# Performance work log

Hardware: AMD Instinct MI355X
Metric: run time of the kernel (lower is better)

Reference implementation:

```python
import jax, jax.numpy as jnp
import numpy as np

T, N, HID = 128, 128, 64
H_, W_ = 8, 8
CONV_OUT = H_ * W_ * HID  # 4096
N_SUB = 5
A, B, C = 5, 3, 6          # subtask_space = task_space.nvec[0]
SUB_SIZE = A + B + C       # 14
N_G = A * B * C            # 90
STATE = N_SUB + SUB_SIZE + HID + SUB_SIZE + 1 + 1  # 99
D_IN = CONV_OUT + 3 * N_SUB  # 4111


def setup_inputs() -> dict:
    key = jax.random.key(0)
    ks = jax.random.split(key, 16)
    sc = 0.02
    obs = jax.random.normal(ks[0], (T, N, CONV_OUT), jnp.float32)
    task_type = jax.random.randint(ks[1], (T, N, N_SUB), 0, A).astype(jnp.float32)
    count = jax.random.randint(ks[2], (T, N, N_SUB), 1, B + 1).astype(jnp.float32)
    obj = jax.random.randint(ks[3], (T, N, N_SUB), 0, C).astype(jnp.float32)
    inp = jnp.concatenate([obs, task_type, count, obj], axis=-1)  # [T,N,4111]
    hx = jnp.zeros((1, N, STATE), jnp.float32)
    return {
        "input": inp,
        "hx": hx,
        "Wf": jax.random.normal(ks[4], (HID, CONV_OUT + 2 * SUB_SIZE + 1), jnp.float32) * sc,
        "bf": jnp.zeros((HID,), jnp.float32),
        "Wih": jax.random.normal(ks[5], (3 * HID, 2 * HID), jnp.float32) * sc,
        "bih": jnp.zeros((3 * HID,), jnp.float32),
        "bhh": jnp.zeros((3 * HID,), jnp.float32),
        "Wc": jax.random.normal(ks[6], (1, 2 * HID), jnp.float32) * sc,
        "bc": jnp.zeros((1,), jnp.float32),
        "Wl": jax.random.normal(ks[7], (3, HID), jnp.float32) * sc,
        "bl": jnp.zeros((3,), jnp.float32),
        "Wpi": jax.random.normal(ks[8], (N_G, HID + SUB_SIZE), jnp.float32) * sc,
        "bpi": jnp.zeros((N_G,), jnp.float32),
        "Wb": jax.random.normal(ks[9], (2, CONV_OUT + SUB_SIZE), jnp.float32) * sc,
        "bb": jnp.zeros((2,), jnp.float32),
    }


def _forward(input, hx, Wf, bf, Wih, bih, bhh, Wc, bc, Wl, bl, Wpi, bpi, Wb, bb):
    obs = input[..., :CONV_OUT]
    tt = input[..., CONV_OUT:CONV_OUT + N_SUB].astype(jnp.int32)
    cnt = input[..., CONV_OUT + N_SUB:CONV_OUT + 2 * N_SUB].astype(jnp.int32) - 1
    obj = input[..., CONV_OUT + 2 * N_SUB:].astype(jnp.int32)

    ea, eb, ec = jnp.eye(A, dtype=input.dtype), jnp.eye(B, dtype=input.dtype), jnp.eye(C, dtype=input.dtype)

    def embed(t1, t2, t3):
        return jnp.concatenate([ea[t1], eb[t2], ec[t3]], axis=-1)

    M = embed(tt[0], cnt[0], obj[0])  # [N, N_SUB, SUB_SIZE]

    # parse hidden state
    h0_all = hx[0]
    i0, i1, i2, i3, i4 = np.cumsum([N_SUB, SUB_SIZE, HID, SUB_SIZE, 1])
    p0, r0, h0, g0, b0 = (h0_all[:, :i0], h0_all[:, i0:i1], h0_all[:, i1:i2],
                          h0_all[:, i2:i3], h0_all[:, i3:i4])

    new_ep = jnp.all(hx == 0)
    p0 = jnp.where(new_ep, p0.at[:, 0].set(1.0), p0)
    r0 = jnp.where(new_ep, M[:, 0], r0)
    g0 = jnp.where(new_ep, M[:, 0], g0)

    bhr, bhz, bhn = jnp.split(bhh, 3)
    keys = jax.random.split(jax.random.key(42), input.shape[0])

    def step(carry, xs):
        p_, r_, h_, g_, bprev = carry
        x, k = xs
        s = jnp.concatenate([x, r_, g_, bprev], axis=-1) @ Wf.T + bf   # f (linear)
        sh = jnp.concatenate([s, h_], axis=-1)
        cg = jax.nn.sigmoid(sh @ Wc.T + bc)                             # [N,1] phi_update
        # GRUCell called with hidden=None -> zero hidden state
        gi = sh @ Wih.T + bih
        gr, gz, gn = jnp.split(gi, 3, axis=-1)
        rg = jax.nn.sigmoid(gr + bhr)
        z = jax.nn.sigmoid(gz + bhz)
        n = jnp.tanh(gn + rg * bhn)
        hnew = (1.0 - z) * n
        # shift attention: per-batch conv1d(p, l, padding=1)
        l = jax.nn.softmax(h_ @ Wl.T + bl, axis=-1)                     # [N,3]
        pp = jnp.pad(p_, ((0, 0), (1, 1)))
        pconv = pp[:, :-2] * l[:, :1] + pp[:, 1:-1] * l[:, 1:2] + pp[:, 2:] * l[:, 2:]
        rnew = jnp.einsum('nk,nks->ns', pconv, M)
        p = cg * pconv + (1.0 - cg) * p_
        r = cg * rnew + (1.0 - cg) * r_
        h = cg * hnew + (1.0 - cg) * h_
        # pi_theta categorical over prod(subtask_space)
        lg = jnp.concatenate([h, r], axis=-1) @ Wpi.T + bpi
        k1, k2 = jax.random.split(k)
        g_idx = jax.random.categorical(k1, lg)                          # [N]
        lp_g = jnp.take_along_axis(jax.nn.log_softmax(lg, axis=-1), g_idx[:, None], axis=1)
        t1 = g_idx // (B * C)
        rem = g_idx % (B * C)
        gemb = embed(t1, rem // C, rem % C)                             # [N, SUB_SIZE]
        g = cg * gemb + (1.0 - cg) * g_
        # beta categorical over 2
        lbeta = jnp.concatenate([x, g], axis=-1) @ Wb.T + bb
        b_idx = jax.random.categorical(k2, lbeta)
        lp_b = jnp.take_along_axis(jax.nn.log_softmax(lbeta, axis=-1), b_idx[:, None], axis=1)
        bflt = b_idx[:, None].astype(p.dtype)
        out = jnp.concatenate([p, r, h, g, bflt, lp_g + lp_b], axis=-1)  # [N, STATE]
        return (p, r, h, g, bflt), out

    _, outs = jax.lax.scan(step, (p0, r0, h0, g0, b0), (obs, keys))
    return outs  # [T, N, STATE]


def reference(input, hx, Wf, bf, Wih, bih, bhh, Wc, bc, Wl, bl, Wpi, bpi, Wb, bb):
    outs = _forward(input, hx, Wf, bf, Wih, bih, bhh, Wc, bc, Wl, bl, Wpi, bpi, Wb, bb)
    return outs, outs[-1]
```

## Files before the change

kernel.cpp:

```cpp
#include <hip/hip_runtime.h>
#include <stdint.h>
#include <math.h>

#define T_STEPS 128
#define NB      128
#define HID     64
#define CONVOUT 4096
#define NSUB    5
#define SUBSZ   14
#define NG      90
#define STATE   99
#define DIN     4111
#define WFCOLS  4125
#define WBCOLS  4110
#define NROWS   (T_STEPS * NB)

__device__ __forceinline__ void tf2x32(unsigned k0, unsigned k1,
                                       unsigned x0, unsigned x1,
                                       unsigned &o0, unsigned &o1) {
  unsigned K0 = k0, K1 = k1, K2 = k0 ^ k1 ^ 0x1BD11BDAu;
  x0 += K0; x1 += K1;
  const int R0[4] = {13, 15, 26, 6};
  const int R1[4] = {17, 29, 16, 24};
  #pragma unroll
  for (int j = 0; j < 4; ++j) { x0 += x1; x1 = (x1 << R0[j]) | (x1 >> (32 - R0[j])); x1 ^= x0; }
  x0 += K1; x1 += K2 + 1u;
  #pragma unroll
  for (int j = 0; j < 4; ++j) { x0 += x1; x1 = (x1 << R1[j]) | (x1 >> (32 - R1[j])); x1 ^= x0; }
  x0 += K2; x1 += K0 + 2u;
  #pragma unroll
  for (int j = 0; j < 4; ++j) { x0 += x1; x1 = (x1 << R0[j]) | (x1 >> (32 - R0[j])); x1 ^= x0; }
  x0 += K0; x1 += K1 + 3u;
  #pragma unroll
  for (int j = 0; j < 4; ++j) { x0 += x1; x1 = (x1 << R1[j]) | (x1 >> (32 - R1[j])); x1 ^= x0; }
  x0 += K1; x1 += K2 + 4u;
  #pragma unroll
  for (int j = 0; j < 4; ++j) { x0 += x1; x1 = (x1 << R0[j]) | (x1 >> (32 - R0[j])); x1 ^= x0; }
  x0 += K2; x1 += K0 + 5u;
  o0 = x0; o1 = x1;
}

__device__ __forceinline__ double bits_to_gumbel_d(unsigned bits) {
  float f = __uint_as_float((bits >> 9) | 0x3f800000u) - 1.0f;
  const double tiny = (double)1.17549435e-38f;
  double u = fmax(tiny, (double)f + tiny);
  return -log(-log(u));
}

__device__ __forceinline__ float rlane(float v, int l) {
  return __int_as_float(__builtin_amdgcn_readlane(__float_as_int(v), l));
}

__device__ __forceinline__ void bar_lds() {
  __asm__ volatile("" ::: "memory");
  __builtin_amdgcn_s_waitcnt(0xC07F);
  __builtin_amdgcn_s_barrier();
  __asm__ volatile("" ::: "memory");
}

__global__ void k_transpose(const float* __restrict__ Wf, const float* __restrict__ Wb,
                            float* __restrict__ Wt) {
  int idx = blockIdx.x * 256 + threadIdx.x;
  int c = idx >> 12;
  int k = idx & 4095;
  float v = (c < 64) ? Wf[(size_t)c * WFCOLS + k] : Wb[(size_t)(c - 64) * WBCOLS + k];
  Wt[(size_t)k * 68 + c] = v;
}

__global__ __launch_bounds__(256, 4) void k_gemm(const float* __restrict__ inp,
                                                 const float* __restrict__ Wt,
                                                 float* __restrict__ Pf,
                                                 double* __restrict__ Pd) {
  __shared__ __align__(16) float xs[64 * 132];
  __shared__ double redd[2][64][2];
  int tid = threadIdx.x;
  int r = tid & 63;
  int w = __builtin_amdgcn_readfirstlane(tid >> 6);
  int rg = blockIdx.x >> 2, kq = blockIdx.x & 3;
  int rowbase = rg * 64;

  float acc[64];
  #pragma unroll
  for (int c = 0; c < 64; ++c) acc[c] = 0.f;
  double ad0 = 0.0, ad1 = 0.0;

  int s_rr[8], s_c4[8];
  #pragma unroll
  for (int i = 0; i < 8; ++i) {
    int idx = tid + i * 256;
    s_rr[i] = idx >> 5;
    s_c4[i] = idx & 31;
  }

  for (int kt = 0; kt < 8; ++kt) {
    int kb = kq * 1024 + kt * 128;
    #pragma unroll
    for (int i = 0; i < 8; ++i) {
      const float* g = inp + (size_t)(rowbase + s_rr[i]) * DIN + kb + s_c4[i] * 4;
      float4 v;
      v.x = g[0]; v.y = g[1]; v.z = g[2]; v.w = g[3];
      *(float4*)&xs[s_rr[i] * 132 + s_c4[i] * 4] = v;
    }
    __syncthreads();
    const float* wkbase = Wt + (size_t)(kb + w * 32) * 68;
    #pragma unroll
    for (int kk = 0; kk < 8; ++kk) {
      float4 xv = *(const float4*)&xs[r * 132 + w * 32 + kk * 4];
      #pragma unroll
      for (int j = 0; j < 4; ++j) {
        float x = (j == 0) ? xv.x : (j == 1) ? xv.y : (j == 2) ? xv.z : xv.w;
        const float* wp = wkbase + (size_t)(kk * 4 + j) * 68;
        #pragma unroll
        for (int c = 0; c < 64; ++c) acc[c] = fmaf(x, wp[c], acc[c]);
        double xd = (double)x;
        ad0 = fma(xd, (double)wp[64], ad0);
        ad1 = fma(xd, (double)wp[65], ad1);
      }
    }
    __syncthreads();
  }

  float* red = xs;
  if (w >= 2) {
    float* d = red + ((size_t)(w - 2) * 64 + r) * 65;
    #pragma unroll
    for (int c = 0; c < 64; ++c) d[c] = acc[c];
    redd[w - 2][r][0] = ad0; redd[w - 2][r][1] = ad1;
  }
  __syncthreads();
  if (w < 2) {
    const float* s = red + ((size_t)w * 64 + r) * 65;
    #pragma unroll
    for (int c = 0; c < 64; ++c) acc[c] += s[c];
    ad0 += redd[w][r][0]; ad1 += redd[w][r][1];
  }
  __syncthreads();
  if (w == 1) {
    float* d = red + (size_t)r * 65;
    #pragma unroll
    for (int c = 0; c < 64; ++c) d[c] = acc[c];
    redd[0][r][0] = ad0; redd[0][r][1] = ad1;
  }
  __syncthreads();
  if (w == 0) {
    const float* s = red + (size_t)r * 65;
    #pragma unroll
    for (int c = 0; c < 64; ++c) acc[c] += s[c];
    ad0 += redd[0][r][0]; ad1 += redd[0][r][1];
    int row = rowbase + r;
    float* po = Pf + (size_t)kq * NROWS * 64 + (size_t)row * 64;
    #pragma unroll
    for (int c = 0; c < 64; ++c) po[c] = acc[c];
    Pd[(size_t)kq * NROWS * 2 + (size_t)row * 2 + 0] = ad0;
    Pd[(size_t)kq * NROWS * 2 + (size_t)row * 2 + 1] = ad1;
  }
}

__global__ void k_reduce(const float* __restrict__ Pf, const double* __restrict__ Pd,
                         float* __restrict__ Xf, double* __restrict__ Xb) {
  size_t gid = (size_t)blockIdx.x * 256 + threadIdx.x;
  const size_t NF = (size_t)NROWS * 64;
  if (gid < NF) {
    Xf[gid] = (Pf[gid] + Pf[NF + gid]) + (Pf[2 * NF + gid] + Pf[3 * NF + gid]);
  } else if (gid < NF + (size_t)NROWS * 2) {
    size_t j = gid - NF;
    const size_t ND = (size_t)NROWS * 2;
    Xb[j] = (Pd[j] + Pd[ND + j]) + (Pd[2 * ND + j] + Pd[3 * ND + j]);
  }
}

__global__ void k_noise(double* __restrict__ Gg, double* __restrict__ Gb) {
  int t = blockIdx.x, tid = threadIdx.x;
  unsigned a, b, k1a, k1b, k2a, k2b, o0, o1;
  tf2x32(0u, 42u, 0u, (unsigned)t, a, b);
  tf2x32(a, b, 0u, 0u, k1a, k1b);
  tf2x32(a, b, 0u, 1u, k2a, k2b);
  for (int i = tid; i < NB * NG; i += 256) {
    tf2x32(k1a, k1b, 0u, (unsigned)i, o0, o1);
    Gg[(size_t)t * NB * NG + i] = bits_to_gumbel_d(o0 ^ o1);
  }
  {
    int i = tid;
    tf2x32(k2a, k2b, 0u, (unsigned)i, o0, o1);
    Gb[(size_t)t * NB * 2 + i] = bits_to_gumbel_d(o0 ^ o1);
  }
}

__global__ __launch_bounds__(256) void k_scan(
    const float* __restrict__ inp, const float* __restrict__ hx,
    const float* __restrict__ Wf, const float* __restrict__ bf,
    const float* __restrict__ Wih, const float* __restrict__ bih,
    const float* __restrict__ bhh, const float* __restrict__ Wc,
    const float* __restrict__ bc, const float* __restrict__ Wl,
    const float* __restrict__ bl, const float* __restrict__ Wpi,
    const float* __restrict__ bpi, const float* __restrict__ Wb,
    const float* __restrict__ bb,
    const float* __restrict__ Xf, const double* __restrict__ Xb,
    const double* __restrict__ Gg, const double* __restrict__ Gb,
    float* __restrict__ lgst, float* __restrict__ lbst,
    int* __restrict__ gidxst, int* __restrict__ bidxst,
    float* __restrict__ out) {
  const int n = blockIdx.x;
  const int tid = threadIdx.x;
  const int lane = tid & 63;
  const int w = __builtin_amdgcn_readfirstlane(tid >> 6);

  __shared__ float s_lds[64], h_lds[64], gi_lds[192];
  __shared__ int nz_sh;

  float wih_r[128];
  float bih_r = 0.f;
  if (w != 0) {
    int m = tid - 64;
    #pragma unroll
    for (int k = 0; k < 128; ++k) wih_r[k] = Wih[(size_t)m * 128 + k];
    bih_r = bih[m];
  }

  float wfs[29], wpi0[78], wpi1[78], mtr[5];
  float bf_r = 0, bhr_r = 0, bhz_r = 0, bhn_r = 0;
  float wc0 = 0, wc1 = 0, wl0 = 0, wl1 = 0, wl2 = 0;
  float bl0 = 0, bl1 = 0, bl2 = 0, bc0 = 0, bpi0 = 0, bpi1 = 0;
  float wbs0 = 0, wbs1 = 0;
  float hreg = 0.f, rgbp = 0.f, xf = 0.f;
  double S0 = 0.0, S1 = 0.0, bb0d = 0.0, bb1d = 0.0;
  double gum0 = 0.0, gum1 = 0.0, xb0 = 0.0, xb1 = 0.0, gb0 = 0.0, gb1 = 0.0;
  int dsto = -1;

  if (tid == 0) nz_sh = 0;
  __syncthreads();
  {
    int any = 0;
    const float4* h4 = (const float4*)hx;
    for (int i = tid; i < (NB * STATE) / 4; i += 256) {
      float4 v = h4[i];
      any |= (v.x != 0.f) | (v.y != 0.f) | (v.z != 0.f) | (v.w != 0.f);
    }
    if (any) nz_sh = 1;
  }
  if (w == 0) {
    #pragma unroll
    for (int k = 0; k < 29; ++k) wfs[k] = Wf[(size_t)lane * WFCOLS + CONVOUT + k];
    #pragma unroll
    for (int k = 0; k < 78; ++k) wpi0[k] = Wpi[(size_t)lane * 78 + k];
    bpi0 = bpi[lane];
    if (lane < 26) {
      #pragma unroll
      for (int k = 0; k < 78; ++k) wpi1[k] = Wpi[(size_t)(64 + lane) * 78 + k];
      bpi1 = bpi[64 + lane];
    }
    bf_r = bf[lane];
    bhr_r = bhh[lane]; bhz_r = bhh[64 + lane]; bhn_r = bhh[128 + lane];
    wc0 = Wc[lane]; wc1 = Wc[64 + lane]; bc0 = bc[0];
    wl0 = Wl[lane]; wl1 = Wl[64 + lane]; wl2 = Wl[128 + lane];
    bl0 = bl[0]; bl1 = bl[1]; bl2 = bl[2];
    bb0d = (double)bb[0]; bb1d = (double)bb[1];
    if (lane < 14) { wbs0 = Wb[CONVOUT + lane]; wbs1 = Wb[(size_t)WBCOLS + CONVOUT + lane]; }
    const float* r0 = inp + (size_t)n * DIN + CONVOUT;
    #pragma unroll
    for (int k = 0; k < 5; ++k) {
      int ttv = (int)r0[k], cntv = (int)r0[5 + k] - 1, objv = (int)r0[10 + k];
      float v = 0.f;
      if (lane < 5)       v = (lane == ttv) ? 1.f : 0.f;
      else if (lane < 8)  v = ((lane - 5) == cntv) ? 1.f : 0.f;
      else if (lane < 14) v = ((lane - 8) == objv) ? 1.f : 0.f;
      mtr[k] = v;
    }
    int src = -1;
    if (lane < 14)       { dsto = 5 + lane;          src = dsto; }
    else if (lane < 28)  { dsto = 83 + (lane - 14);  src = dsto; }
    else if (lane == 28) { dsto = 97;                src = 97; }
    else if (lane < 34)  { dsto = lane - 29;         src = dsto; }
    rgbp = (src >= 0) ? hx[(size_t)n * STATE + src] : 0.f;
    hreg = hx[(size_t)n * STATE + 19 + lane];
  }
  __syncthreads();
  if (w == 0) {
    if (nz_sh == 0) {
      const float* r0 = inp + (size_t)n * DIN + CONVOUT;
      int tt0 = (int)r0[0], cnt0 = (int)r0[5] - 1, obj0 = (int)r0[10];
      if (lane == 29) rgbp = 1.f;
      else if (lane < 14) rgbp = mtr[0];
      else if (lane >= 14 && lane < 28) {
        int j = lane - 14;
        rgbp = (j < 5) ? ((j == tt0) ? 1.f : 0.f)
             : (j < 8) ? (((j - 5) == cnt0) ? 1.f : 0.f)
                       : (((j - 8) == obj0) ? 1.f : 0.f);
      }
    }
    #pragma unroll
    for (int j = 0; j < 14; ++j) {
      double gv = (double)rlane(rgbp, 14 + j);
      S0 += gv * (double)rlane(wbs0, j);
      S1 += gv * (double)rlane(wbs1, j);
    }
    h_lds[lane] = hreg;
    gum0 = Gg[(size_t)n * NG + lane];
    gum1 = (lane < 26) ? Gg[(size_t)n * NG + 64 + lane] : 0.0;
    xf = Xf[(size_t)n * 64 + lane];
    xb0 = Xb[(size_t)n * 2 + 0]; xb1 = Xb[(size_t)n * 2 + 1];
    gb0 = Gb[(size_t)n * 2 + 0]; gb1 = Gb[(size_t)n * 2 + 1];
  }
  __syncthreads();

  const size_t outF = (size_t)T_STEPS * NB * STATE;

  #pragma unroll 1
  for (int t = 0; t < T_STEPS; ++t) {
    float sv_own = 0.f, cg = 0.f, accR0 = 0.f, accR1 = 0.f;
    double cgd = 0.0;

    if (w == 0) {
      float acc = xf + bf_r;
      #pragma unroll
      for (int k = 0; k < 29; ++k) acc = fmaf(wfs[k], rlane(rgbp, k), acc);
      sv_own = acc;
      s_lds[lane] = acc;
    }
    bar_lds();

    if (w == 0) {
      float p0 = wl0 * hreg, p1 = wl1 * hreg, p2 = wl2 * hreg;
      float cga = fmaf(wc1, hreg, wc0 * sv_own);
      #pragma unroll
      for (int off = 32; off; off >>= 1) {
        p0 += __shfl_xor(p0, off, 64);
        p1 += __shfl_xor(p1, off, 64);
        p2 += __shfl_xor(p2, off, 64);
        cga += __shfl_xor(cga, off, 64);
      }
      p0 += bl0; p1 += bl1; p2 += bl2;
      float mx = fmaxf(p0, fmaxf(p1, p2));
      float e0 = expf(p0 - mx), e1 = expf(p1 - mx), e2 = expf(p2 - mx);
      float se = e0 + e1 + e2;
      float l0 = e0 / se, l1 = e1 / se, l2 = e2 / se;
      cg = 1.f / (1.f + expf(-(cga + bc0)));
      cgd = (double)cg;
      float pv0 = rlane(rgbp, 29), pv1 = rlane(rgbp, 30), pv2 = rlane(rgbp, 31);
      float pv3 = rlane(rgbp, 32), pv4 = rlane(rgbp, 33);
      float pc0 = pv0 * l1 + pv1 * l2;
      float pc1 = pv0 * l0 + pv1 * l1 + pv2 * l2;
      float pc2 = pv1 * l0 + pv2 * l1 + pv3 * l2;
      float pc3 = pv2 * l0 + pv3 * l1 + pv4 * l2;
      float pc4 = pv3 * l0 + pv4 * l1;
      if (lane >= 29 && lane < 34) {
        float pcl = (lane == 29) ? pc0 : (lane == 30) ? pc1 : (lane == 31) ? pc2
                  : (lane == 32) ? pc3 : pc4;
        rgbp = cg * pcl + (1.f - cg) * rgbp;
      }
      if (lane < 14) {
        float rn = pc0 * mtr[0] + pc1 * mtr[1] + pc2 * mtr[2] + pc3 * mtr[3] + pc4 * mtr[4];
        rgbp = cg * rn + (1.f - cg) * rgbp;
      }
      #pragma unroll
      for (int k = 0; k < 14; ++k) {
        float rv = rlane(rgbp, k);
        accR0 = fmaf(wpi0[64 + k], rv, accR0);
        accR1 = fmaf(wpi1[64 + k], rv, accR1);
      }
    } else {
      float sv = s_lds[lane];
      float hv = h_lds[lane];
      float acc = bih_r;
      #pragma unroll
      for (int k = 0; k < 64; ++k) acc = fmaf(wih_r[k], rlane(sv, k), acc);
      #pragma unroll
      for (int k = 0; k < 64; ++k) acc = fmaf(wih_r[64 + k], rlane(hv, k), acc);
      gi_lds[tid - 64] = acc;
    }
    bar_lds();

    if (w == 0) {
      int tn = (t + 1 < T_STEPS) ? t + 1 : t;
      double gum0n = Gg[(size_t)tn * NB * NG + (size_t)n * NG + lane];
      double gum1n = (lane < 26) ? Gg[(size_t)tn * NB * NG + (size_t)n * NG + 64 + lane] : 0.0;
      float xfn = Xf[((size_t)tn * NB + n) * 64 + lane];
      double xb0n = Xb[((size_t)tn * NB + n) * 2 + 0];
      double xb1n = Xb[((size_t)tn * NB + n) * 2 + 1];
      double gb0n = Gb[((size_t)tn * NB + n) * 2 + 0];
      double gb1n = Gb[((size_t)tn * NB + n) * 2 + 1];

      float g0 = gi_lds[lane], g1 = gi_lds[64 + lane], g2 = gi_lds[128 + lane];
      float rg = 1.f / (1.f + expf(-(g0 + bhr_r)));
      float z  = 1.f / (1.f + expf(-(g1 + bhz_r)));
      float nn = tanhf(g2 + rg * bhn_r);
      float hnew = (1.f - z) * nn;
      hreg = cg * hnew + (1.f - cg) * hreg;

      float a0 = bpi0 + accR0, a1 = bpi1 + accR1;
      #pragma unroll
      for (int k = 0; k < 64; ++k) {
        float hv2 = rlane(hreg, k);
        a0 = fmaf(wpi0[k], hv2, a0);
        a1 = fmaf(wpi1[k], hv2, a1);
      }
      const float NEGINF = -3.0e38f;
      float vb0 = (float)(gum0 + (double)a0);
      float vb1 = (lane < 26) ? (float)(gum1 + (double)a1) : NEGINF;
      float m1, m2; int idx;
      if (vb1 > vb0) { m1 = vb1; idx = lane + 64; m2 = vb0; }
      else           { m1 = vb0; idx = lane;      m2 = vb1; }
      #pragma unroll
      for (int off = 32; off; off >>= 1) {
        float o1 = __shfl_xor(m1, off, 64);
        int   oi = __shfl_xor(idx, off, 64);
        float o2 = __shfl_xor(m2, off, 64);
        bool take = (o1 > m1) || (o1 == m1 && oi < idx);
        float base2 = take ? m1 : m2;
        float oth   = take ? o2 : o1;
        m2 = fmaxf(base2, oth);
        if (take) { m1 = o1; idx = oi; }
      }
      int gidx = idx;
      if (m1 - m2 < 3e-5f) {
        double e0d = (double)bpi0;
        double e1d = (lane < 26) ? (double)bpi1 : -1.0e300;
        #pragma unroll 1
        for (int k = 0; k < 64; ++k) {
          double hv2 = (double)rlane(hreg, k);
          e0d = fma((double)Wpi[(size_t)lane * 78 + k], hv2, e0d);
          if (lane < 26) e1d = fma((double)Wpi[(size_t)(64 + lane) * 78 + k], hv2, e1d);
        }
        #pragma unroll 1
        for (int k = 0; k < 14; ++k) {
          double rv = (double)rlane(rgbp, k);
          e0d = fma((double)Wpi[(size_t)lane * 78 + 64 + k], rv, e0d);
          if (lane < 26) e1d = fma((double)Wpi[(size_t)(64 + lane) * 78 + 64 + k], rv, e1d);
        }
        double kk0 = e0d + gum0;
        double kk1 = (lane < 26) ? e1d + gum1 : -1.0e300;
        double d1; int di;
        if (kk1 > kk0) { d1 = kk1; di = lane + 64; } else { d1 = kk0; di = lane; }
        #pragma unroll
        for (int off = 32; off; off >>= 1) {
          double od = __shfl_xor(d1, off, 64);
          int    oi = __shfl_xor(di, off, 64);
          if (od > d1 || (od == d1 && oi < di)) { d1 = od; di = oi; }
        }
        gidx = di;
      }
      int t1 = gidx / 18, rem = gidx - t1 * 18;
      int b1 = rem / 6, c1 = rem - b1 * 6;
      if (lane >= 14 && lane < 28) {
        int j = lane - 14;
        float ge = (j < 5) ? ((j == t1) ? 1.f : 0.f)
                 : (j < 8) ? (((j - 5) == b1) ? 1.f : 0.f)
                           : (((j - 8) == c1) ? 1.f : 0.f);
        rgbp = cg * ge + (1.f - cg) * rgbp;
      }
      double u0 = (double)rlane(wbs0, t1) + (double)rlane(wbs0, 5 + b1) + (double)rlane(wbs0, 8 + c1);
      double u1 = (double)rlane(wbs1, t1) + (double)rlane(wbs1, 5 + b1) + (double)rlane(wbs1, 8 + c1);
      S0 = cgd * u0 + (1.0 - cgd) * S0;
      S1 = cgd * u1 + (1.0 - cgd) * S1;
      double lb0 = xb0 + bb0d + S0;
      double lb1 = xb1 + bb1d + S1;
      int bi = ((lb1 + gb1) > (lb0 + gb0)) ? 1 : 0;
      if (lane == 28) rgbp = (float)bi;

      size_t rn = (size_t)t * NB + n;
      float* ob = out + rn * STATE;
      if (dsto >= 0) ob[dsto] = rgbp;
      ob[19 + lane] = hreg;
      lgst[rn * NG + lane] = a0;
      if (lane < 26) lgst[rn * NG + 64 + lane] = a1;
      if (lane == 0) {
        lbst[rn * 2 + 0] = (float)lb0; lbst[rn * 2 + 1] = (float)lb1;
        gidxst[rn] = gidx; bidxst[rn] = bi;
      }
      if (t == T_STEPS - 1) {
        float* of = out + outF + (size_t)n * STATE;
        if (dsto >= 0) of[dsto] = rgbp;
        of[19 + lane] = hreg;
      }
      h_lds[lane] = hreg;
      gum0 = gum0n; gum1 = gum1n; xf = xfn;
      xb0 = xb0n; xb1 = xb1n; gb0 = gb0n; gb1 = gb1n;
    }
  }
}

__global__ __launch_bounds__(256) void k_lp(const float* __restrict__ lgst,
                                            const float* __restrict__ lbst,
                                            const int* __restrict__ gidxst,
                                            const int* __restrict__ bidxst,
                                            float* __restrict__ out) {
  int tid = threadIdx.x, lane = tid & 63, w = tid >> 6;
  size_t rn = (size_t)blockIdx.x * 4 + w;
  const float* lg = lgst + rn * NG;
  float v0 = lg[lane];
  float v1 = (lane < 26) ? lg[64 + lane] : -3.0e38f;
  float ml = fmaxf(v0, v1);
  #pragma unroll
  for (int off = 32; off; off >>= 1) ml = fmaxf(ml, __shfl_xor(ml, off, 64));
  float e = expf(v0 - ml) + ((lane < 26) ? expf(v1 - ml) : 0.f);
  #pragma unroll
  for (int off = 32; off; off >>= 1) e += __shfl_xor(e, off, 64);
  int gi = gidxst[rn];
  float lpg = (lg[gi] - ml) - logf(e);
  float lb0 = lbst[rn * 2 + 0], lb1 = lbst[rn * 2 + 1];
  int bi = bidxst[rn];
  float mx = fmaxf(lb0, lb1);
  float seb = expf(lb0 - mx) + expf(lb1 - mx);
  float lpb = ((bi ? lb1 : lb0) - mx) - logf(seb);
  if (lane == 0) {
    int t = (int)(rn / NB), n = (int)(rn % NB);
    float lp = lpg + lpb;
    out[rn * STATE + 98] = lp;
    if (t == T_STEPS - 1) out[(size_t)T_STEPS * NB * STATE + (size_t)n * STATE + 98] = lp;
  }
}

extern "C" void kernel_launch(void* const* d_in, const int* in_sizes, int n_in,
                              void* d_out, int out_size, void* d_ws, size_t ws_size,
                              hipStream_t stream) {
  const float* inp = (const float*)d_in[0];
  const float* hx  = (const float*)d_in[1];
  const float* Wf  = (const float*)d_in[2];
  const float* bf  = (const float*)d_in[3];
  const float* Wih = (const float*)d_in[4];
  const float* bih = (const float*)d_in[5];
  const float* bhh = (const float*)d_in[6];
  const float* Wc  = (const float*)d_in[7];
  const float* bc  = (const float*)d_in[8];
  const float* Wl  = (const float*)d_in[9];
  const float* bl  = (const float*)d_in[10];
  const float* Wpi = (const float*)d_in[11];
  const float* bpi = (const float*)d_in[12];
  const float* Wb  = (const float*)d_in[13];
  const float* bb  = (const float*)d_in[14];
  float* out = (float*)d_out;

  double* Gg = (double*)d_ws;
  double* Gb = Gg + (size_t)T_STEPS * NB * NG;
  double* Xb = Gb + (size_t)T_STEPS * NB * 2;
  double* Pd = Xb + (size_t)NROWS * 2;
  float*  Wt = (float*)(Pd + (size_t)4 * NROWS * 2);
  float*  Xf = Wt + (size_t)4096 * 68;
  float*  Pf = Xf + (size_t)NROWS * 64;
  float*  lgst = Pf;
  float*  lbst = lgst + (size_t)NROWS * NG;
  int*    gidxst = (int*)(lbst + (size_t)NROWS * 2);
  int*    bidxst = gidxst + NROWS;

  k_transpose<<<(66 * 4096) / 256, 256, 0, stream>>>(Wf, Wb, Wt);
  k_gemm<<<1024, 256, 0, stream>>>(inp, Wt, Pf, Pd);
  {
    size_t tot = (size_t)NROWS * 64 + (size_t)NROWS * 2;
    k_reduce<<<(int)((tot + 255) / 256), 256, 0, stream>>>(Pf, Pd, Xf, Xb);
  }
  k_noise<<<T_STEPS, 256, 0, stream>>>(Gg, Gb);
  k_scan<<<NB, 256, 0, stream>>>(inp, hx, Wf, bf, Wih, bih, bhh, Wc, bc, Wl, bl,
                                 Wpi, bpi, Wb, bb, Xf, Xb, Gg, Gb,
                                 lgst, lbst, gidxst, bidxst, out);
  k_lp<<<NROWS / 4, 256, 0, stream>>>(lgst, lbst, gidxst, bidxst, out);
}
```

Measured before the change: 963.0 us.

## Incrementally update recurrent input projections and use DPP reductions in sequential kernel

Result: faster. 834.4 us (-13.4%).

```diff
diff --git a/kernel.cpp b/kernel.cpp
--- a/kernel.cpp
+++ b/kernel.cpp
@@ -15,6 +15,10 @@
 #define WBCOLS  4110
 #define NROWS   (T_STEPS * NB)
 
+#define NEGINFF (-3.0e38f)
+
+typedef __attribute__((ext_vector_type(2))) float f32x2;
+
 __device__ __forceinline__ void tf2x32(unsigned k0, unsigned k1,
                                        unsigned x0, unsigned x1,
                                        unsigned &o0, unsigned &o1) {
@@ -49,6 +53,12 @@
 
 __device__ __forceinline__ float rlane(float v, int l) {
   return __int_as_float(__builtin_amdgcn_readlane(__float_as_int(v), l));
+}
+
+template<int CTRL, int RM>
+__device__ __forceinline__ float dpp_mv(float x, float fill) {
+  return __int_as_float(__builtin_amdgcn_update_dpp(
+      __float_as_int(fill), __float_as_int(x), CTRL, RM, 0xF, false));
 }
 
 __device__ __forceinline__ void bar_lds() {
@@ -205,27 +215,39 @@
   const int lane = tid & 63;
   const int w = __builtin_amdgcn_readfirstlane(tid >> 6);
 
-  __shared__ float s_lds[64], h_lds[64], gi_lds[192];
+  __shared__ __align__(16) float sh_lds[128];
+  __shared__ float gi_lds[192];
   __shared__ int nz_sh;
 
-  float wih_r[128];
+  f32x2 wih_p[64];
   float bih_r = 0.f;
   if (w != 0) {
     int m = tid - 64;
-    #pragma unroll
-    for (int k = 0; k < 128; ++k) wih_r[k] = Wih[(size_t)m * 128 + k];
+    const f32x2* wrow = (const f32x2*)&Wih[(size_t)m * 128];
+    #pragma unroll
+    for (int k2 = 0; k2 < 64; ++k2) wih_p[k2] = wrow[k2];
     bih_r = bih[m];
   }
 
-  float wfs[29], wpi0[78], wpi1[78], mtr[5];
+  f32x2 wpi0_p[32], wpi1_p[32];
+  float wfsg[14], mtr[5], WfrM[5], WpiM0[5], WpiM1[5];
+  float wfs28 = 0.f;
   float bf_r = 0, bhr_r = 0, bhz_r = 0, bhn_r = 0;
   float wc0 = 0, wc1 = 0, wl0 = 0, wl1 = 0, wl2 = 0;
   float bl0 = 0, bl1 = 0, bl2 = 0, bc0 = 0, bpi0 = 0, bpi1 = 0;
   float wbs0 = 0, wbs1 = 0;
-  float hreg = 0.f, rgbp = 0.f, xf = 0.f;
+  float hreg = 0.f, rgbp = 0.f;
+  float sv_own = 0.f, R_s = 0.f, G_s = 0.f;
+  float accR0_run = 0.f, accR1_run = 0.f;
+  float xfp = 0.f;
   double S0 = 0.0, S1 = 0.0, bb0d = 0.0, bb1d = 0.0;
   double gum0 = 0.0, gum1 = 0.0, xb0 = 0.0, xb1 = 0.0, gb0 = 0.0, gb1 = 0.0;
   int dsto = -1;
+
+  #pragma unroll
+  for (int k = 0; k < 5; ++k) { mtr[k] = 0.f; WfrM[k] = 0.f; WpiM0[k] = 0.f; WpiM1[k] = 0.f; }
+  #pragma unroll
+  for (int k = 0; k < 14; ++k) wfsg[k] = 0.f;
 
   if (tid == 0) nz_sh = 0;
   __syncthreads();
@@ -239,16 +261,19 @@
     if (any) nz_sh = 1;
   }
   if (w == 0) {
-    #pragma unroll
-    for (int k = 0; k < 29; ++k) wfs[k] = Wf[(size_t)lane * WFCOLS + CONVOUT + k];
-    #pragma unroll
-    for (int k = 0; k < 78; ++k) wpi0[k] = Wpi[(size_t)lane * 78 + k];
+    const f32x2* w0row = (const f32x2*)&Wpi[(size_t)lane * 78];
+    #pragma unroll
+    for (int k2 = 0; k2 < 32; ++k2) wpi0_p[k2] = w0row[k2];
     bpi0 = bpi[lane];
     if (lane < 26) {
+      const f32x2* w1row = (const f32x2*)&Wpi[(size_t)(64 + lane) * 78];
       #pragma unroll
-      for (int k = 0; k < 78; ++k) wpi1[k] = Wpi[(size_t)(64 + lane) * 78 + k];
+      for (int k2 = 0; k2 < 32; ++k2) wpi1_p[k2] = w1row[k2];
       bpi1 = bpi[64 + lane];
     }
+    #pragma unroll
+    for (int k = 0; k < 14; ++k) wfsg[k] = Wf[(size_t)lane * WFCOLS + CONVOUT + 14 + k];
+    wfs28 = Wf[(size_t)lane * WFCOLS + CONVOUT + 28];
     bf_r = bf[lane];
     bhr_r = bhh[lane]; bhz_r = bhh[64 + lane]; bhn_r = bhh[128 + lane];
     wc0 = Wc[lane]; wc1 = Wc[64 + lane]; bc0 = bc[0];
@@ -265,6 +290,14 @@
       else if (lane < 8)  v = ((lane - 5) == cntv) ? 1.f : 0.f;
       else if (lane < 14) v = ((lane - 8) == objv) ? 1.f : 0.f;
       mtr[k] = v;
+      const float* wfr = Wf + (size_t)lane * WFCOLS + CONVOUT;
+      WfrM[k] = wfr[ttv] + wfr[5 + cntv] + wfr[8 + objv];
+      const float* wp0 = Wpi + (size_t)lane * 78 + 64;
+      WpiM0[k] = wp0[ttv] + wp0[5 + cntv] + wp0[8 + objv];
+      if (lane < 26) {
+        const float* wp1 = Wpi + (size_t)(64 + lane) * 78 + 64;
+        WpiM1[k] = wp1[ttv] + wp1[5 + cntv] + wp1[8 + objv];
+      }
     }
     int src = -1;
     if (lane < 14)       { dsto = 5 + lane;          src = dsto; }
@@ -294,12 +327,27 @@
       S0 += gv * (double)rlane(wbs0, j);
       S1 += gv * (double)rlane(wbs1, j);
     }
-    h_lds[lane] = hreg;
+    R_s = 0.f; accR0_run = 0.f; accR1_run = 0.f;
+    #pragma unroll
+    for (int j = 0; j < 14; ++j) {
+      float rv = rlane(rgbp, j);
+      R_s = fmaf(Wf[(size_t)lane * WFCOLS + CONVOUT + j], rv, R_s);
+      accR0_run = fmaf(Wpi[(size_t)lane * 78 + 64 + j], rv, accR0_run);
+      if (lane < 26) accR1_run = fmaf(Wpi[(size_t)(64 + lane) * 78 + 64 + j], rv, accR1_run);
+    }
+    G_s = 0.f;
+    #pragma unroll
+    for (int j = 0; j < 14; ++j) G_s = fmaf(wfsg[j], rlane(rgbp, 14 + j), G_s);
+    float b0v = rlane(rgbp, 28);
+    float xf0 = Xf[(size_t)n * 64 + lane];
     gum0 = Gg[(size_t)n * NG + lane];
     gum1 = (lane < 26) ? Gg[(size_t)n * NG + 64 + lane] : 0.0;
-    xf = Xf[(size_t)n * 64 + lane];
     xb0 = Xb[(size_t)n * 2 + 0]; xb1 = Xb[(size_t)n * 2 + 1];
     gb0 = Gb[(size_t)n * 2 + 0]; gb1 = Gb[(size_t)n * 2 + 1];
+    sv_own = xf0 + bf_r + R_s + G_s + b0v * wfs28;
+    sh_lds[lane] = sv_own;
+    sh_lds[64 + lane] = hreg;
+    xfp = Xf[((size_t)((T_STEPS > 1) ? 1 : 0) * NB + n) * 64 + lane];
   }
   __syncthreads();
 
@@ -307,34 +355,25 @@
 
   #pragma unroll 1
   for (int t = 0; t < T_STEPS; ++t) {
-    float sv_own = 0.f, cg = 0.f, accR0 = 0.f, accR1 = 0.f;
+    float cg = 0.f;
     double cgd = 0.0;
-
-    if (w == 0) {
-      float acc = xf + bf_r;
-      #pragma unroll
-      for (int k = 0; k < 29; ++k) acc = fmaf(wfs[k], rlane(rgbp, k), acc);
-      sv_own = acc;
-      s_lds[lane] = acc;
-    }
-    bar_lds();
 
     if (w == 0) {
       float p0 = wl0 * hreg, p1 = wl1 * hreg, p2 = wl2 * hreg;
       float cga = fmaf(wc1, hreg, wc0 * sv_own);
-      #pragma unroll
-      for (int off = 32; off; off >>= 1) {
-        p0 += __shfl_xor(p0, off, 64);
-        p1 += __shfl_xor(p1, off, 64);
-        p2 += __shfl_xor(p2, off, 64);
-        cga += __shfl_xor(cga, off, 64);
-      }
-      p0 += bl0; p1 += bl1; p2 += bl2;
-      float mx = fmaxf(p0, fmaxf(p1, p2));
-      float e0 = expf(p0 - mx), e1 = expf(p1 - mx), e2 = expf(p2 - mx);
+      #define DPP_SUM4(C, RM) \
+        { p0 += dpp_mv<C,RM>(p0, 0.f); p1 += dpp_mv<C,RM>(p1, 0.f); \
+          p2 += dpp_mv<C,RM>(p2, 0.f); cga += dpp_mv<C,RM>(cga, 0.f); }
+      DPP_SUM4(0x111, 0xF) DPP_SUM4(0x112, 0xF) DPP_SUM4(0x114, 0xF)
+      DPP_SUM4(0x118, 0xF) DPP_SUM4(0x142, 0xA) DPP_SUM4(0x143, 0xC)
+      #undef DPP_SUM4
+      float P0 = rlane(p0, 63) + bl0, P1 = rlane(p1, 63) + bl1, P2 = rlane(p2, 63) + bl2;
+      float CGA = rlane(cga, 63);
+      float mx = fmaxf(P0, fmaxf(P1, P2));
+      float e0 = expf(P0 - mx), e1 = expf(P1 - mx), e2 = expf(P2 - mx);
       float se = e0 + e1 + e2;
       float l0 = e0 / se, l1 = e1 / se, l2 = e2 / se;
-      cg = 1.f / (1.f + expf(-(cga + bc0)));
+      cg = 1.f / (1.f + expf(-(CGA + bc0)));
       cgd = (double)cg;
       float pv0 = rlane(rgbp, 29), pv1 = rlane(rgbp, 30), pv2 = rlane(rgbp, 31);
       float pv3 = rlane(rgbp, 32), pv4 = rlane(rgbp, 33);
@@ -352,29 +391,32 @@
         float rn = pc0 * mtr[0] + pc1 * mtr[1] + pc2 * mtr[2] + pc3 * mtr[3] + pc4 * mtr[4];
         rgbp = cg * rn + (1.f - cg) * rgbp;
       }
+      float rd0 = pc0 * WpiM0[0] + pc1 * WpiM0[1] + pc2 * WpiM0[2] + pc3 * WpiM0[3] + pc4 * WpiM0[4];
+      accR0_run = cg * rd0 + (1.f - cg) * accR0_run;
+      float rd1 = pc0 * WpiM1[0] + pc1 * WpiM1[1] + pc2 * WpiM1[2] + pc3 * WpiM1[3] + pc4 * WpiM1[4];
+      accR1_run = cg * rd1 + (1.f - cg) * accR1_run;
+      float rfd = pc0 * WfrM[0] + pc1 * WfrM[1] + pc2 * WfrM[2] + pc3 * WfrM[3] + pc4 * WfrM[4];
+      R_s = cg * rfd + (1.f - cg) * R_s;
+    } else {
+      const f32x2* shp = (const f32x2*)sh_lds;
+      f32x2 acc0 = {bih_r, 0.f}, acc1 = {0.f, 0.f};
       #pragma unroll
-      for (int k = 0; k < 14; ++k) {
-        float rv = rlane(rgbp, k);
-        accR0 = fmaf(wpi0[64 + k], rv, accR0);
-        accR1 = fmaf(wpi1[64 + k], rv, accR1);
-      }
-    } else {
-      float sv = s_lds[lane];
-      float hv = h_lds[lane];
-      float acc = bih_r;
-      #pragma unroll
-      for (int k = 0; k < 64; ++k) acc = fmaf(wih_r[k], rlane(sv, k), acc);
-      #pragma unroll
-      for (int k = 0; k < 64; ++k) acc = fmaf(wih_r[64 + k], rlane(hv, k), acc);
-      gi_lds[tid - 64] = acc;
+      for (int k2 = 0; k2 < 64; k2 += 2) {
+        f32x2 v0 = shp[k2], v1 = shp[k2 + 1];
+        acc0.x = fmaf(wih_p[k2].x,     v0.x, acc0.x);
+        acc0.y = fmaf(wih_p[k2].y,     v0.y, acc0.y);
+        acc1.x = fmaf(wih_p[k2 + 1].x, v1.x, acc1.x);
+        acc1.y = fmaf(wih_p[k2 + 1].y, v1.y, acc1.y);
+      }
+      gi_lds[tid - 64] = (acc0.x + acc0.y) + (acc1.x + acc1.y);
     }
     bar_lds();
 
     if (w == 0) {
       int tn = (t + 1 < T_STEPS) ? t + 1 : t;
+      int tpp = (t + 2 < T_STEPS) ? t + 2 : T_STEPS - 1;
       double gum0n = Gg[(size_t)tn * NB * NG + (size_t)n * NG + lane];
       double gum1n = (lane < 26) ? Gg[(size_t)tn * NB * NG + (size_t)n * NG + 64 + lane] : 0.0;
-      float xfn = Xf[((size_t)tn * NB + n) * 64 + lane];
       double xb0n = Xb[((size_t)tn * NB + n) * 2 + 0];
       double xb1n = Xb[((size_t)tn * NB + n) * 2 + 1];
       double gb0n = Gb[((size_t)tn * NB + n) * 2 + 0];
@@ -386,33 +428,40 @@
       float nn = tanhf(g2 + rg * bhn_r);
       float hnew = (1.f - z) * nn;
       hreg = cg * hnew + (1.f - cg) * hreg;
-
-      float a0 = bpi0 + accR0, a1 = bpi1 + accR1;
+      sh_lds[64 + lane] = hreg;
+
+      const f32x2* hp = (const f32x2*)&sh_lds[64];
+      f32x2 A0 = {bpi0 + accR0_run, 0.f}, B0 = {0.f, 0.f};
+      f32x2 A1 = {bpi1 + accR1_run, 0.f}, B1 = {0.f, 0.f};
       #pragma unroll
-      for (int k = 0; k < 64; ++k) {
-        float hv2 = rlane(hreg, k);
-        a0 = fmaf(wpi0[k], hv2, a0);
-        a1 = fmaf(wpi1[k], hv2, a1);
-      }
-      const float NEGINF = -3.0e38f;
+      for (int k2 = 0; k2 < 32; k2 += 2) {
+        f32x2 h0 = hp[k2], h1 = hp[k2 + 1];
+        A0.x = fmaf(wpi0_p[k2].x,     h0.x, A0.x);
+        A0.y = fmaf(wpi0_p[k2].y,     h0.y, A0.y);
+        B0.x = fmaf(wpi0_p[k2 + 1].x, h1.x, B0.x);
+        B0.y = fmaf(wpi0_p[k2 + 1].y, h1.y, B0.y);
+        A1.x = fmaf(wpi1_p[k2].x,     h0.x, A1.x);
+        A1.y = fmaf(wpi1_p[k2].y,     h0.y, A1.y);
+        B1.x = fmaf(wpi1_p[k2 + 1].x, h1.x, B1.x);
+        B1.y = fmaf(wpi1_p[k2 + 1].y, h1.y, B1.y);
+      }
+      float a0 = (A0.x + A0.y) + (B0.x + B0.y);
+      float a1 = (A1.x + A1.y) + (B1.x + B1.y);
+
       float vb0 = (float)(gum0 + (double)a0);
-      float vb1 = (lane < 26) ? (float)(gum1 + (double)a1) : NEGINF;
-      float m1, m2; int idx;
-      if (vb1 > vb0) { m1 = vb1; idx = lane + 64; m2 = vb0; }
-      else           { m1 = vb0; idx = lane;      m2 = vb1; }
-      #pragma unroll
-      for (int off = 32; off; off >>= 1) {
-        float o1 = __shfl_xor(m1, off, 64);
-        int   oi = __shfl_xor(idx, off, 64);
-        float o2 = __shfl_xor(m2, off, 64);
-        bool take = (o1 > m1) || (o1 == m1 && oi < idx);
-        float base2 = take ? m1 : m2;
-        float oth   = take ? o2 : o1;
-        m2 = fmaxf(base2, oth);
-        if (take) { m1 = o1; idx = oi; }
-      }
-      int gidx = idx;
-      if (m1 - m2 < 3e-5f) {
+      float vb1 = (lane < 26) ? (float)(gum1 + (double)a1) : NEGINFF;
+      float m1 = fmaxf(vb0, vb1), m2 = fminf(vb0, vb1);
+      #define DPP_AMAX(C, RM) \
+        { float o1 = dpp_mv<C,RM>(m1, NEGINFF), o2 = dpp_mv<C,RM>(m2, NEGINFF); \
+          m2 = fmaxf(m2, fmaxf(o2, fminf(m1, o1))); m1 = fmaxf(m1, o1); }
+      DPP_AMAX(0x111, 0xF) DPP_AMAX(0x112, 0xF) DPP_AMAX(0x114, 0xF)
+      DPP_AMAX(0x118, 0xF) DPP_AMAX(0x142, 0xA) DPP_AMAX(0x143, 0xC)
+      #undef DPP_AMAX
+      float M1 = rlane(m1, 63), M2 = rlane(m2, 63);
+      unsigned long long bm0 = __ballot(vb0 == M1);
+      unsigned long long bm1 = __ballot(vb1 == M1);
+      int gidx = bm0 ? (__ffsll(bm0) - 1) : (64 + __ffsll(bm1) - 1);
+      if (M1 - M2 < 3e-5f) {
         double e0d = (double)bpi0;
         double e1d = (lane < 26) ? (double)bpi1 : -1.0e300;
         #pragma unroll 1
@@ -448,6 +497,12 @@
                            : (((j - 8) == c1) ? 1.f : 0.f);
         rgbp = cg * ge + (1.f - cg) * rgbp;
       }
+      float gt = (t1 == 0) ? wfsg[0] : (t1 == 1) ? wfsg[1] : (t1 == 2) ? wfsg[2]
+               : (t1 == 3) ? wfsg[3] : wfsg[4];
+      float gbv = (b1 == 0) ? wfsg[5] : (b1 == 1) ? wfsg[6] : wfsg[7];
+      float gcv = (c1 == 0) ? wfsg[8] : (c1 == 1) ? wfsg[9] : (c1 == 2) ? wfsg[10]
+               : (c1 == 3) ? wfsg[11] : (c1 == 4) ? wfsg[12] : wfsg[13];
+      G_s = cg * (gt + gbv + gcv) + (1.f - cg) * G_s;
       double u0 = (double)rlane(wbs0, t1) + (double)rlane(wbs0, 5 + b1) + (double)rlane(wbs0, 8 + c1);
       double u1 = (double)rlane(wbs1, t1) + (double)rlane(wbs1, 5 + b1) + (double)rlane(wbs1, 8 + c1);
       S0 = cgd * u0 + (1.0 - cgd) * S0;
@@ -456,6 +511,11 @@
       double lb1 = xb1 + bb1d + S1;
       int bi = ((lb1 + gb1) > (lb0 + gb0)) ? 1 : 0;
       if (lane == 28) rgbp = (float)bi;
+
+      float Bv = bi ? wfs28 : 0.f;
+      sv_own = xfp + bf_r + (R_s + G_s) + Bv;
+      sh_lds[lane] = sv_own;
+      xfp = Xf[((size_t)tpp * NB + n) * 64 + lane];
 
       size_t rn = (size_t)t * NB + n;
       float* ob = out + rn * STATE;
@@ -472,10 +532,10 @@
         if (dsto >= 0) of[dsto] = rgbp;
         of[19 + lane] = hreg;
       }
-      h_lds[lane] = hreg;
-      gum0 = gum0n; gum1 = gum1n; xf = xfn;
+      gum0 = gum0n; gum1 = gum1n;
       xb0 = xb0n; xb1 = xb1n; gb0 = gb0n; gb1 = gb1n;
     }
+    bar_lds();
   }
 }
 
```
